# Performance work log

Hardware: AMD Instinct MI355X
Metric: run time of the kernel (lower is better)

## Reference

```python
import jax, jax.numpy as jnp
import numpy as np

B, S, HID = 4, 1024, 4096
H, HKV, D = 32, 8, 128
R = 16
THETA = 10000.0
LORA_SCALE = 1.0


def setup_inputs() -> dict:
    key = jax.random.key(0)
    ks = jax.random.split(key, 13)
    w = 0.02  # init scale for stability
    return {
        "hidden_states": jax.random.normal(ks[0], (B, S, HID), jnp.float32),
        "Wq": jax.random.normal(ks[1], (H * D, HID), jnp.float32) * w,
        "Wk": jax.random.normal(ks[2], (HKV * D, HID), jnp.float32) * w,
        "Wv": jax.random.normal(ks[3], (HKV * D, HID), jnp.float32) * w,
        "Wo": jax.random.normal(ks[4], (HID, H * D), jnp.float32) * w,
        "Aq": jax.random.normal(ks[5], (B, R, HID), jnp.float32) * w,
        "Bq": jax.random.normal(ks[6], (B, H * D, R), jnp.float32) * w,
        "Ak": jax.random.normal(ks[7], (B, R, HID), jnp.float32) * w,
        "Bk": jax.random.normal(ks[8], (B, HKV * D, R), jnp.float32) * w,
        "Av": jax.random.normal(ks[9], (B, R, HID), jnp.float32) * w,
        "Bv": jax.random.normal(ks[10], (B, HKV * D, R), jnp.float32) * w,
        "Ao": jax.random.normal(ks[11], (B, R, H * D), jnp.float32) * w,
        "Bo": jax.random.normal(ks[12], (B, HID, R), jnp.float32) * w,
    }


def _lora(x, A, Bm):
    # per-request (batched) LoRA: x:[B,S,in], A:[B,r,in], Bm:[B,out,r]
    t = jnp.einsum("bsi,bri->bsr", x, A)
    return jnp.einsum("bsr,bor->bso", t, Bm) * LORA_SCALE


def _rope_tables(seq_len, head_dim, theta):
    inv_freq = 1.0 / (theta ** (jnp.arange(0, head_dim, 2, dtype=jnp.float32) / head_dim))
    ang = jnp.arange(seq_len, dtype=jnp.float32)[:, None] * inv_freq[None, :]  # [S, D/2]
    return jnp.cos(ang), jnp.sin(ang)


def _apply_rope(x, cos, sin):
    # x: [B,S,h,D]; cos/sin: [S,D/2]
    x1, x2 = jnp.split(x, 2, axis=-1)
    c = cos[None, :, None, :]
    s = sin[None, :, None, :]
    return jnp.concatenate([x1 * c - x2 * s, x2 * c + x1 * s], axis=-1)


def reference(hidden_states, Wq, Wk, Wv, Wo, Aq, Bq, Ak, Bk, Av, Bv, Ao, Bo):
    x = hidden_states
    # base projections + batched LoRA deltas (apply_lora_weight_kvq)
    q = x @ Wq.T + _lora(x, Aq, Bq)                 # [B,S,H*D]
    k = x @ Wk.T + _lora(x, Ak, Bk)                 # [B,S,HKV*D]
    v = x @ Wv.T + _lora(x, Av, Bv)

    q = q.reshape(B, S, H, D)
    k = k.reshape(B, S, HKV, D)
    v = v.reshape(B, S, HKV, D)

    cos, sin = _rope_tables(S, D, THETA)
    q = _apply_rope(q, cos, sin)
    k = _apply_rope(k, cos, sin)

    # GQA: repeat kv heads to match q heads
    rep = H // HKV
    k = jnp.repeat(k, rep, axis=2)                  # [B,S,H,D]
    v = jnp.repeat(v, rep, axis=2)

    scores = jnp.einsum("bqhd,bkhd->bhqk", q, k) / jnp.sqrt(jnp.float32(D))
    causal = jnp.tril(jnp.ones((S, S), dtype=bool))
    scores = jnp.where(causal[None, None], scores, jnp.finfo(scores.dtype).min)
    probs = jax.nn.softmax(scores, axis=-1)
    attn_raw = jnp.einsum("bhqk,bkhd->bqhd", probs, v).reshape(B, S, H * D)

    # out projection + batched LoRA on attn (apply_lora_weight_attn uses attn_raw)
    out = attn_raw @ Wo.T + _lora(attn_raw, Ao, Bo)  # [B,S,HID]
    return out
```

## Files before the change

kernel.cpp:

```cpp
#include <hip/hip_runtime.h>

typedef unsigned short u16;
typedef __attribute__((ext_vector_type(8))) short short8;
typedef __attribute__((ext_vector_type(4))) float f32x4;

#define BB 4
#define SS 1024
#define HIDN 4096
#define HH 32
#define HKV 8
#define DD 128
#define RR 16
#define MM (BB * SS)
#define NQKV 6144

__device__ __forceinline__ u16 f2bf(float f) {
    unsigned u = __builtin_bit_cast(unsigned, f);
    unsigned r = u + 0x7FFFu + ((u >> 16) & 1u);
    return (u16)(r >> 16);
}
__device__ __forceinline__ float bf2f(u16 u) {
    unsigned v = ((unsigned)u) << 16;
    return __builtin_bit_cast(float, v);
}
__device__ __forceinline__ void glds16(const u16* g, u16* l) {
    __builtin_amdgcn_global_load_lds((const __attribute__((address_space(1))) unsigned int*)g,
                                     (__attribute__((address_space(3))) unsigned int*)l, 16, 0, 0);
}

__global__ void zero_kernel(float* __restrict__ p, int n) {
    int i = blockIdx.x * blockDim.x + threadIdx.x;
    if (i < n) p[i] = 0.f;
}

__global__ void cast_kernel(const float* __restrict__ src, u16* __restrict__ dst, int n4) {
    int i = blockIdx.x * blockDim.x + threadIdx.x;
    int stride = gridDim.x * blockDim.x;
    for (; i < n4; i += stride) {
        float4 v = reinterpret_cast<const float4*>(src)[i];
        ushort4 o;
        o.x = f2bf(v.x); o.y = f2bf(v.y); o.z = f2bf(v.z); o.w = f2bf(v.w);
        reinterpret_cast<ushort4*>(dst)[i] = o;
    }
}

__global__ void cast_lora_a(const float* __restrict__ src, u16* __restrict__ dst,
                            int perB4, int dstStrideU16, int n4) {
    int i = blockIdx.x * blockDim.x + threadIdx.x;
    int stride = gridDim.x * blockDim.x;
    for (; i < n4; i += stride) {
        int b = i / perB4;
        int w4 = i - b * perB4;
        float4 v = reinterpret_cast<const float4*>(src)[i];
        ushort4 o;
        o.x = f2bf(v.x); o.y = f2bf(v.y); o.z = f2bf(v.z); o.w = f2bf(v.w);
        reinterpret_cast<ushort4*>(dst + (size_t)b * dstStrideU16)[w4] = o;
    }
}

template <int NT>
__global__ __launch_bounds__(256) void lora_mfma(
        const u16* __restrict__ Xb, const u16* __restrict__ Ab, float* __restrict__ T) {
    const int N = NT * 16;
    __shared__ __attribute__((aligned(16))) u16 Xls[128 * 32];
    __shared__ __attribute__((aligned(16))) u16 Als[NT * 16 * 32];
    int tid = threadIdx.x;
    int wave = tid >> 6, lane = tid & 63;
    int quad = lane >> 4, l15 = lane & 15;
    int m0 = blockIdx.y * 128;
    int b = m0 >> 10;
    int k0base = blockIdx.x * (HIDN / 4);
    const u16* Abb = Ab + (size_t)b * N * HIDN;
    f32x4 acc[2][NT] = {};
    int r0 = tid >> 2;
    int c0 = (tid & 3) * 8;
    for (int k0 = k0base; k0 < k0base + HIDN / 4; k0 += 32) {
        *(uint4*)&Xls[r0 * 32 + c0]        = *(const uint4*)&Xb[(size_t)(m0 + r0) * HIDN + k0 + c0];
        *(uint4*)&Xls[(r0 + 64) * 32 + c0] = *(const uint4*)&Xb[(size_t)(m0 + r0 + 64) * HIDN + k0 + c0];
        if (tid < NT * 16 * 4)
            *(uint4*)&Als[r0 * 32 + c0] = *(const uint4*)&Abb[(size_t)r0 * HIDN + k0 + c0];
        __syncthreads();
        short8 xf[2], af[NT];
#pragma unroll
        for (int mi = 0; mi < 2; mi++)
            xf[mi] = *(const short8*)&Xls[(wave * 32 + mi * 16 + l15) * 32 + quad * 8];
#pragma unroll
        for (int nt = 0; nt < NT; nt++)
            af[nt] = *(const short8*)&Als[(nt * 16 + l15) * 32 + quad * 8];
#pragma unroll
        for (int mi = 0; mi < 2; mi++)
#pragma unroll
            for (int nt = 0; nt < NT; nt++)
                acc[mi][nt] = __builtin_amdgcn_mfma_f32_16x16x32_bf16(xf[mi], af[nt], acc[mi][nt], 0, 0, 0);
        __syncthreads();
    }
#pragma unroll
    for (int mi = 0; mi < 2; mi++)
#pragma unroll
        for (int nt = 0; nt < NT; nt++)
#pragma unroll
            for (int r = 0; r < 4; r++) {
                int row = m0 + wave * 32 + mi * 16 + quad * 4 + r;
                atomicAdd(&T[(size_t)row * N + nt * 16 + l15], acc[mi][nt][r]);
            }
}

__global__ __launch_bounds__(256) void gemm_fused(
        const u16* __restrict__ Xb, const u16* __restrict__ Wb,
        const float* __restrict__ T, int tstride,
        const float* __restrict__ Bl0, const float* __restrict__ Bl1, const float* __restrict__ Bl2,
        int ns0, int ns1, int ns2, int secb0, int secb1,
        void* __restrict__ outp, int Nout, int out_f32) {
    const int K = HIDN;
    __shared__ __attribute__((aligned(16))) u16 Als[128 * 32];
    __shared__ __attribute__((aligned(16))) u16 Bls[128 * 32];
    int tid = threadIdx.x;
    int wave = tid >> 6, lane = tid & 63;
    int quad = lane >> 4, l15 = lane & 15;
    int wm = wave >> 1, wn = wave & 1;
    int m0 = blockIdx.y * 128, n0 = blockIdx.x * 128;
    int b = m0 >> 10;

    int sec = (n0 >= secb0) + (n0 >= secb1);
    const float* Blp = (sec == 0) ? Bl0 : ((sec == 1) ? Bl1 : Bl2);
    int nsec = (sec == 0) ? ns0 : ((sec == 1) ? ns1 : ns2);
    int colbase = (sec == 0) ? 0 : ((sec == 1) ? secb0 : secb1);
    int toff = sec * 16;
    const float* BlB = Blp + (size_t)b * nsec * RR;

    f32x4 acc[4][4] = {};
    int arow = wave * 32 + (lane >> 2);
    int achunk = ((lane & 3) ^ ((lane >> 3) & 3)) * 8;
    const u16* gA0 = &Xb[(size_t)(m0 + arow) * K + achunk];
    const u16* gA1 = gA0 + (size_t)16 * K;
    const u16* gB0 = &Wb[(size_t)(n0 + arow) * K + achunk];
    const u16* gB1 = gB0 + (size_t)16 * K;
    u16* lA0 = &Als[wave * 32 * 32];
    u16* lA1 = &Als[(wave * 32 + 16) * 32];
    u16* lB0 = &Bls[wave * 32 * 32];
    u16* lB1 = &Bls[(wave * 32 + 16) * 32];
    int sel = ((l15 >> 1) & 3);

    auto compute = [&]() {
        short8 af[4], bfr[4];
#pragma unroll
        for (int mi = 0; mi < 4; mi++)
            af[mi] = *(const short8*)&Als[(wm * 64 + mi * 16 + l15) * 32 + ((quad ^ sel) * 8)];
#pragma unroll
        for (int ni = 0; ni < 4; ni++)
            bfr[ni] = *(const short8*)&Bls[(wn * 64 + ni * 16 + l15) * 32 + ((quad ^ sel) * 8)];
#pragma unroll
        for (int mi = 0; mi < 4; mi++)
#pragma unroll
            for (int ni = 0; ni < 4; ni++)
                acc[mi][ni] = __builtin_amdgcn_mfma_f32_16x16x32_bf16(af[mi], bfr[ni], acc[mi][ni], 0, 0, 0);
    };

    for (int k0 = 0; k0 < K; k0 += 32) {
        glds16(gA0 + k0, lA0);
        glds16(gA1 + k0, lA1);
        glds16(gB0 + k0, lB0);
        glds16(gB1 + k0, lB1);
        __syncthreads();
        compute();
        __syncthreads();
    }

    {
        int r = tid >> 1;
        int s = (r >> 1) & 3;
        short8 z = {0, 0, 0, 0, 0, 0, 0, 0};
        if ((tid & 1) == 0) {
            const float* Tr = &T[(size_t)(m0 + r) * tstride + toff];
            short8 c0v, c1v;
#pragma unroll
            for (int e = 0; e < 4; e++) {
                c0v[e]     = (short)f2bf(Tr[e]);
                c0v[e + 4] = (short)f2bf(Tr[4 + e]);
                c1v[e]     = (short)f2bf(Tr[8 + e]);
                c1v[e + 4] = (short)f2bf(Tr[12 + e]);
            }
            *(short8*)&Als[r * 32 + (0 ^ s) * 8] = c0v;
            *(short8*)&Als[r * 32 + (1 ^ s) * 8] = c1v;
            *(short8*)&Als[r * 32 + (2 ^ s) * 8] = z;
            *(short8*)&Als[r * 32 + (3 ^ s) * 8] = z;
        } else {
            const float* Br = &BlB[(size_t)(n0 - colbase + r) * RR];
            short8 c0v, c1v;
#pragma unroll
            for (int e = 0; e < 4; e++) {
                c0v[e]     = (short)f2bf(Br[e]);
                c0v[e + 4] = (short)f2bf(Br[4 + e]);
                c1v[e]     = (short)f2bf(Br[8 + e]);
                c1v[e + 4] = (short)f2bf(Br[12 + e]);
            }
            *(short8*)&Bls[r * 32 + (0 ^ s) * 8] = c0v;
            *(short8*)&Bls[r * 32 + (1 ^ s) * 8] = c1v;
            *(short8*)&Bls[r * 32 + (2 ^ s) * 8] = z;
            *(short8*)&Bls[r * 32 + (3 ^ s) * 8] = z;
        }
    }
    __syncthreads();
    compute();

#pragma unroll
    for (int mi = 0; mi < 4; mi++) {
#pragma unroll
        for (int r = 0; r < 4; r++) {
            int row = m0 + wm * 64 + mi * 16 + quad * 4 + r;
#pragma unroll
            for (int ni = 0; ni < 4; ni++) {
                int col = n0 + wn * 64 + ni * 16 + l15;
                float v = acc[mi][ni][r];
                if (out_f32) ((float*)outp)[(size_t)row * Nout + col] = v;
                else         ((u16*)outp)[(size_t)row * Nout + col]  = f2bf(v);
            }
        }
    }
}

__global__ void rope_kernel(u16* __restrict__ x, int lognh, int rowstride, int total) {
    int idx = blockIdx.x * 256 + threadIdx.x;
    if (idx >= total) return;
    int d = idx & 63;
    int t = idx >> 6;
    int h = t & ((1 << lognh) - 1);
    int row = t >> lognh;
    int pos = row & (SS - 1);
    size_t base = (size_t)row * rowstride + h * DD;
    float inv = __expf(-(float)d * (9.210340371976184f / 64.0f));
    float ang = (float)pos * inv;
    float c = cosf(ang), s = sinf(ang);
    float x1 = bf2f(x[base + d]);
    float x2 = bf2f(x[base + 64 + d]);
    x[base + d]      = f2bf(x1 * c - x2 * s);
    x[base + 64 + d] = f2bf(x2 * c + x1 * s);
}

#define KLD 136
#define VTLD 72
#define PLD 72
__global__ __launch_bounds__(256) void flash_kernel(
        const u16* __restrict__ Q, const u16* __restrict__ Kx, const u16* __restrict__ V,
        u16* __restrict__ Oa, int qs, int kvs) {
    __shared__ __attribute__((aligned(16))) u16 Kls[64 * KLD];
    __shared__ __attribute__((aligned(16))) u16 Vt[128 * VTLD];
    __shared__ __attribute__((aligned(16))) u16 Pls[4 * 32 * PLD];
    int tid = threadIdx.x;
    int wave = tid >> 6, lane = tid & 63;
    int quad = lane >> 4, l15 = lane & 15;
    int blk = blockIdx.x;
    int qt = 7 - (blk >> 7);
    int h  = blk & 31;
    int b  = (blk >> 5) & 3;
    int hkv = h >> 2;
    int q0 = qt * 128;
    const float scale = 0.08838834764831845f;

    short8 qf[2][4];
#pragma unroll
    for (int mi = 0; mi < 2; mi++) {
        int qrow = q0 + (wave + 4 * mi) * 16 + l15;
        const u16* qp = Q + (size_t)(b * SS + qrow) * qs + h * DD;
#pragma unroll
        for (int kt = 0; kt < 4; kt++) qf[mi][kt] = *(const short8*)&qp[kt * 32 + quad * 8];
    }

    f32x4 oacc[2][8] = {};
    float mrow[2][4], lrow[2][4];
#pragma unroll
    for (int mi = 0; mi < 2; mi++)
#pragma unroll
        for (int r = 0; r < 4; r++) { mrow[mi][r] = -3.0e38f; lrow[mi][r] = 0.f; }

    int krow = tid >> 2;
    int kc   = (tid & 3) * 32;
    int vp   = tid >> 3;
    int vc   = (tid & 7) * 16;

    int nkb = (q0 >> 6) + 2;
    for (int ib = 0; ib < nkb; ib++) {
        int kb = ib * 64;
        const u16* kg = Kx + (size_t)(b * SS + kb + krow) * kvs + hkv * DD + kc;
#pragma unroll
        for (int j = 0; j < 4; j++)
            *(uint4*)&Kls[krow * KLD + kc + j * 8] = *(const uint4*)&kg[j * 8];
        const u16* vg0 = V + (size_t)(b * SS + kb + 2 * vp) * kvs + hkv * DD + vc;
        const u16* vg1 = vg0 + kvs;
#pragma unroll
        for (int j = 0; j < 2; j++) {
            uint4 a4 = *(const uint4*)&vg0[j * 8];
            uint4 b4 = *(const uint4*)&vg1[j * 8];
            const u16* ap = (const u16*)&a4;
            const u16* bp = (const u16*)&b4;
#pragma unroll
            for (int e = 0; e < 8; e++) {
                unsigned pk = (unsigned)ap[e] | ((unsigned)bp[e] << 16);
                *(unsigned*)&Vt[(size_t)(vc + j * 8 + e) * VTLD + 2 * vp] = pk;
            }
        }
        __syncthreads();

        f32x4 sa[2][4] = {};
#pragma unroll
        for (int nt = 0; nt < 4; nt++) {
            short8 kf[4];
#pragma unroll
            for (int kt = 0; kt < 4; kt++)
                kf[kt] = *(const short8*)&Kls[(nt * 16 + l15) * KLD + kt * 32 + quad * 8];
#pragma unroll
            for (int mi = 0; mi < 2; mi++)
#pragma unroll
                for (int kt = 0; kt < 4; kt++)
                    sa[mi][nt] = __builtin_amdgcn_mfma_f32_16x16x32_bf16(qf[mi][kt], kf[kt], sa[mi][nt], 0, 0, 0);
        }

#pragma unroll
        for (int mi = 0; mi < 2; mi++) {
#pragma unroll
            for (int r = 0; r < 4; r++) {
                int qpos = q0 + (wave + 4 * mi) * 16 + quad * 4 + r;
                float s[4];
#pragma unroll
                for (int nt = 0; nt < 4; nt++) {
                    float v = sa[mi][nt][r] * scale;
                    int kpos = kb + nt * 16 + l15;
                    s[nt] = (kpos > qpos) ? -3.0e38f : v;
                }
                float mx = fmaxf(fmaxf(s[0], s[1]), fmaxf(s[2], s[3]));
#pragma unroll
                for (int off = 1; off < 16; off <<= 1) mx = fmaxf(mx, __shfl_xor(mx, off, 64));
                float mnew = fmaxf(mrow[mi][r], mx);
                float alpha = __expf(mrow[mi][r] - mnew);
                mrow[mi][r] = mnew;
                float sum = 0.f;
#pragma unroll
                for (int nt = 0; nt < 4; nt++) {
                    float e = __expf(s[nt] - mnew);
                    sum += e;
                    Pls[wave * (32 * PLD) + (mi * 16 + quad * 4 + r) * PLD + nt * 16 + l15] = f2bf(e);
                }
#pragma unroll
                for (int off = 1; off < 16; off <<= 1) sum += __shfl_xor(sum, off, 64);
                lrow[mi][r] = lrow[mi][r] * alpha + sum;
#pragma unroll
                for (int dt = 0; dt < 8; dt++) oacc[mi][dt][r] *= alpha;
            }
        }
        __syncthreads();

#pragma unroll
        for (int kt = 0; kt < 2; kt++) {
            short8 pf[2];
#pragma unroll
            for (int mi = 0; mi < 2; mi++)
                pf[mi] = *(const short8*)&Pls[wave * (32 * PLD) + (mi * 16 + l15) * PLD + kt * 32 + quad * 8];
#pragma unroll
            for (int dt = 0; dt < 8; dt++) {
                short8 vf = *(const short8*)&Vt[(size_t)(dt * 16 + l15) * VTLD + kt * 32 + quad * 8];
#pragma unroll
                for (int mi = 0; mi < 2; mi++)
                    oacc[mi][dt] = __builtin_amdgcn_mfma_f32_16x16x32_bf16(pf[mi], vf, oacc[mi][dt], 0, 0, 0);
            }
        }
        __syncthreads();
    }

#pragma unroll
    for (int mi = 0; mi < 2; mi++)
#pragma unroll
        for (int r = 0; r < 4; r++) {
            float inv = 1.0f / lrow[mi][r];
            int orow = q0 + (wave + 4 * mi) * 16 + quad * 4 + r;
            u16* op = Oa + ((size_t)(b * SS + orow) * HH + h) * DD;
#pragma unroll
            for (int dt = 0; dt < 8; dt++)
                op[dt * 16 + l15] = f2bf(oacc[mi][dt][r] * inv);
        }
}

extern "C" void kernel_launch(void* const* d_in, const int* in_sizes, int n_in,
                              void* d_out, int out_size, void* d_ws, size_t ws_size,
                              hipStream_t stream) {
    const float* X  = (const float*)d_in[0];
    const float* Wq = (const float*)d_in[1];
    const float* Wk = (const float*)d_in[2];
    const float* Wv = (const float*)d_in[3];
    const float* Wo = (const float*)d_in[4];
    const float* Aq = (const float*)d_in[5];
    const float* Bq = (const float*)d_in[6];
    const float* Ak = (const float*)d_in[7];
    const float* Bk = (const float*)d_in[8];
    const float* Av = (const float*)d_in[9];
    const float* Bv = (const float*)d_in[10];
    const float* Ao = (const float*)d_in[11];
    const float* Bo = (const float*)d_in[12];

    char* w = (char*)d_ws;
    auto take = [&](size_t bytes) {
        char* p = w;
        w += (bytes + 255) & ~(size_t)255;
        return p;
    };
    u16*   Xb  = (u16*)  take((size_t)MM * HIDN * 2);
    u16*   Wqb = (u16*)  take((size_t)HIDN * HIDN * 2);
    u16*   Wkb = (u16*)  take((size_t)1024 * HIDN * 2);
    u16*   Wvb = (u16*)  take((size_t)1024 * HIDN * 2);
    u16*   Wob = (u16*)  take((size_t)HIDN * HIDN * 2);
    float* Tcat= (float*)take((size_t)MM * 48 * 4);
    float* To  = (float*)take((size_t)MM * 16 * 4);
    u16*   Acat= (u16*)  take((size_t)BB * 48 * HIDN * 2);
    u16*   Aob = (u16*)  take((size_t)BB * 16 * HIDN * 2);
    u16*   qkv = (u16*)  take((size_t)MM * NQKV * 2);
    u16*   attn = Xb;

    (void)Wkb; (void)Wvb;

    zero_kernel<<<(MM * 64 + 255) / 256, 256, 0, stream>>>(Tcat, MM * 64);

    cast_kernel<<<2048, 256, 0, stream>>>(X,  Xb,  MM * HIDN / 4);
    cast_kernel<<<2048, 256, 0, stream>>>(Wq, Wqb, HIDN * HIDN / 4);
    cast_kernel<<<1024, 256, 0, stream>>>(Wk, Wkb, 1024 * HIDN / 4);
    cast_kernel<<<1024, 256, 0, stream>>>(Wv, Wvb, 1024 * HIDN / 4);
    cast_kernel<<<2048, 256, 0, stream>>>(Wo, Wob, HIDN * HIDN / 4);
    {
        const int perB4 = 16 * HIDN / 4;
        const int n4 = BB * perB4;
        cast_lora_a<<<256, 256, 0, stream>>>(Aq, Acat,             perB4, 48 * HIDN, n4);
        cast_lora_a<<<256, 256, 0, stream>>>(Ak, Acat + 16 * HIDN, perB4, 48 * HIDN, n4);
        cast_lora_a<<<256, 256, 0, stream>>>(Av, Acat + 32 * HIDN, perB4, 48 * HIDN, n4);
        cast_kernel<<<256, 256, 0, stream>>>(Ao, Aob, BB * 16 * HIDN / 4);
    }

    lora_mfma<3><<<dim3(4, 32), 256, 0, stream>>>(Xb, Acat, Tcat);

    gemm_fused<<<dim3(48, 32), 256, 0, stream>>>(
        Xb, Wqb, Tcat, 48, Bq, Bk, Bv, HIDN, 1024, 1024, 4096, 5120,
        (void*)qkv, NQKV, 0);

    rope_kernel<<<(BB * SS * HH * 64 + 255) / 256, 256, 0, stream>>>(qkv,        5, NQKV, BB * SS * HH * 64);
    rope_kernel<<<(BB * SS * HKV * 64 + 255) / 256, 256, 0, stream>>>(qkv + 4096, 3, NQKV, BB * SS * HKV * 64);

    flash_kernel<<<BB * HH * (SS / 128), 256, 0, stream>>>(qkv, qkv + 4096, qkv + 5120, attn, NQKV, NQKV);

    lora_mfma<1><<<dim3(4, 32), 256, 0, stream>>>(attn, Aob, To);

    gemm_fused<<<dim3(32, 32), 256, 0, stream>>>(
        attn, Wob, To, 16, Bo, Bo, Bo, HIDN, HIDN, HIDN, 1 << 30, 1 << 30,
        (void*)d_out, HIDN, 1);
}
```

Measured before the change: 898.3 us.

## Replace 128x128 GEMM with double-buffered 256x256 ping-pong pipelined GEMM

Swaps the projection GEMM for a 512-thread kernel with 256x256 tiles, K-step 64, and double-buffered LDS. Global-to-LDS loads for later K tiles are interleaved across eight phases and gated by vmcnt waits and raw s_barrier. MFMA bursts run at raised wave priority. The goal is to hide memory latency and raise data reuse per tile, at the cost of more LDS and registers and fewer blocks (384 and 256) on the GPU.

```diff
diff --git a/kernel.cpp b/kernel.cpp
--- a/kernel.cpp
+++ b/kernel.cpp
@@ -27,6 +27,9 @@
     __builtin_amdgcn_global_load_lds((const __attribute__((address_space(1))) unsigned int*)g,
                                      (__attribute__((address_space(3))) unsigned int*)l, 16, 0, 0);
 }
+
+#define BAR()    asm volatile("s_barrier" ::: "memory")
+#define VMCNT6() asm volatile("s_waitcnt vmcnt(6)" ::: "memory")
 
 __global__ void zero_kernel(float* __restrict__ p, int n) {
     int i = blockIdx.x * blockDim.x + threadIdx.x;
@@ -105,20 +108,51 @@
             }
 }
 
-__global__ __launch_bounds__(256) void gemm_fused(
+#define GPH(DB, MB, NB, LOADA, LOADB, STG, ENDW) do {                                   \
+    if (LOADA) {                                                                        \
+        _Pragma("unroll") for (int q_ = 0; q_ < 4; q_++) {                              \
+            int row_ = wm * 128 + ((MB) + q_) * 16 + l15; int sw_ = row_ & 7;           \
+            _Pragma("unroll") for (int kk_ = 0; kk_ < 2; kk_++)                         \
+                afr[q_][kk_] = *(const short8*)&As[DB][row_][((kk_ * 4 + quad) ^ sw_) * 8]; \
+        }                                                                               \
+    }                                                                                   \
+    if (LOADB) {                                                                        \
+        _Pragma("unroll") for (int j_ = 0; j_ < 2; j_++) {                              \
+            int row_ = wn * 64 + ((NB) + j_) * 16 + l15; int sw_ = row_ & 7;            \
+            _Pragma("unroll") for (int kk_ = 0; kk_ < 2; kk_++)                         \
+                bfr[(NB) + j_][kk_] = *(const short8*)&Bs[DB][row_][((kk_ * 4 + quad) ^ sw_) * 8]; \
+        }                                                                               \
+    }                                                                                   \
+    STG;                                                                                \
+    BAR();                                                                              \
+    asm volatile("s_waitcnt lgkmcnt(0)" ::: "memory");                                  \
+    __builtin_amdgcn_sched_barrier(0);                                                  \
+    __builtin_amdgcn_s_setprio(1);                                                      \
+    _Pragma("unroll") for (int kk_ = 0; kk_ < 2; kk_++)                                 \
+    _Pragma("unroll") for (int q_ = 0; q_ < 4; q_++)                                    \
+    _Pragma("unroll") for (int j_ = 0; j_ < 2; j_++)                                    \
+        acc[(MB) + q_][(NB) + j_] = __builtin_amdgcn_mfma_f32_16x16x32_bf16(            \
+            afr[q_][kk_], bfr[(NB) + j_][kk_], acc[(MB) + q_][(NB) + j_], 0, 0, 0);     \
+    __builtin_amdgcn_s_setprio(0);                                                      \
+    ENDW;                                                                               \
+    BAR();                                                                              \
+} while (0)
+
+__global__ __launch_bounds__(512, 2) void gemm256(
         const u16* __restrict__ Xb, const u16* __restrict__ Wb,
         const float* __restrict__ T, int tstride,
         const float* __restrict__ Bl0, const float* __restrict__ Bl1, const float* __restrict__ Bl2,
         int ns0, int ns1, int ns2, int secb0, int secb1,
         void* __restrict__ outp, int Nout, int out_f32) {
     const int K = HIDN;
-    __shared__ __attribute__((aligned(16))) u16 Als[128 * 32];
-    __shared__ __attribute__((aligned(16))) u16 Bls[128 * 32];
+    const int NKT = K / 64;
+    __shared__ __attribute__((aligned(16))) u16 As[2][256][64];
+    __shared__ __attribute__((aligned(16))) u16 Bs[2][256][64];
     int tid = threadIdx.x;
     int wave = tid >> 6, lane = tid & 63;
     int quad = lane >> 4, l15 = lane & 15;
-    int wm = wave >> 1, wn = wave & 1;
-    int m0 = blockIdx.y * 128, n0 = blockIdx.x * 128;
+    int wm = wave >> 2, wn = wave & 3;
+    int m0 = blockIdx.y * 256, n0 = blockIdx.x * 256;
     int b = m0 >> 10;
 
     int sec = (n0 >= secb0) + (n0 >= secb1);
@@ -128,92 +162,109 @@
     int toff = sec * 16;
     const float* BlB = Blp + (size_t)b * nsec * RR;
 
-    f32x4 acc[4][4] = {};
-    int arow = wave * 32 + (lane >> 2);
-    int achunk = ((lane & 3) ^ ((lane >> 3) & 3)) * 8;
-    const u16* gA0 = &Xb[(size_t)(m0 + arow) * K + achunk];
-    const u16* gA1 = gA0 + (size_t)16 * K;
-    const u16* gB0 = &Wb[(size_t)(n0 + arow) * K + achunk];
-    const u16* gB1 = gB0 + (size_t)16 * K;
-    u16* lA0 = &Als[wave * 32 * 32];
-    u16* lA1 = &Als[(wave * 32 + 16) * 32];
-    u16* lB0 = &Bls[wave * 32 * 32];
-    u16* lB1 = &Bls[(wave * 32 + 16) * 32];
-    int sel = ((l15 >> 1) & 3);
-
-    auto compute = [&]() {
-        short8 af[4], bfr[4];
-#pragma unroll
-        for (int mi = 0; mi < 4; mi++)
-            af[mi] = *(const short8*)&Als[(wm * 64 + mi * 16 + l15) * 32 + ((quad ^ sel) * 8)];
-#pragma unroll
-        for (int ni = 0; ni < 4; ni++)
-            bfr[ni] = *(const short8*)&Bls[(wn * 64 + ni * 16 + l15) * 32 + ((quad ^ sel) * 8)];
-#pragma unroll
-        for (int mi = 0; mi < 4; mi++)
+    int rlo = lane >> 3;
+    int cch = lane & 7;
+    unsigned offA[4]; int lA[4];
+#pragma unroll
+    for (int q = 0; q < 4; q++) {
+        int rb = ((wave & 4) << 5) + q * 32 + (wave & 3) * 8;
+        int r = rb + rlo;
+        int g = cch ^ (r & 7);
+        offA[q] = (unsigned)((m0 + r) * K + g * 8);
+        lA[q] = rb;
+    }
+    unsigned offB[2][2]; int lB[2][2];
+#pragma unroll
+    for (int h = 0; h < 2; h++)
+#pragma unroll
+        for (int j = 0; j < 2; j++) {
+            int u = wave * 2 + j;
+            int rb = (u >> 2) * 64 + (u & 3) * 8 + h * 32;
+            int r = rb + rlo;
+            int g = cch ^ (r & 7);
+            offB[h][j] = (unsigned)((n0 + r) * K + g * 8);
+            lB[h][j] = rb;
+        }
+
+    auto stA = [&](int db, int q, int kofs) { glds16(Xb + offA[q] + kofs, &As[db][lA[q]][0]); };
+    auto stB = [&](int db, int h, int j, int kofs) { glds16(Wb + offB[h][j] + kofs, &Bs[db][lB[h][j]][0]); };
+
+    f32x4 acc[8][4] = {};
+    short8 afr[4][2];
+    short8 bfr[4][2];
+
+    stA(0, 0, 0); stA(0, 1, 0); stB(0, 0, 0, 0); stB(0, 0, 1, 0);
+    stA(0, 2, 0); stA(0, 3, 0); stB(0, 1, 0, 0); stB(0, 1, 1, 0);
+    stA(1, 0, 64); stA(1, 1, 64); stB(1, 0, 0, 64); stB(1, 0, 1, 64);
+    stA(1, 2, 64); stA(1, 3, 64);
+    VMCNT6();
+    BAR();
+
+    for (int it = 0; it < NKT / 2; ++it) {
+        int t2 = 2 * it + 2, t3 = 2 * it + 3;
+        int k1 = (2 * it + 1) * 64;
+        int k2 = (t2 < NKT ? t2 : NKT - 1) * 64;
+        int k3 = (t3 < NKT ? t3 : NKT - 1) * 64;
+
+        GPH(0, 0, 0, 1, 1, { stB(1, 1, 0, k1); stB(1, 1, 1, k1); }, );
+        GPH(0, 0, 2, 0, 1, { stA(0, 0, k2); stA(0, 1, k2); }, );
+        GPH(0, 4, 0, 1, 0, { stB(0, 0, 0, k2); stB(0, 0, 1, k2); }, );
+        GPH(0, 4, 2, 0, 0, { stA(0, 2, k2); stA(0, 3, k2); }, VMCNT6());
+        GPH(1, 0, 0, 1, 1, { stB(0, 1, 0, k2); stB(0, 1, 1, k2); }, );
+        GPH(1, 0, 2, 0, 1, { stA(1, 0, k3); stA(1, 1, k3); }, );
+        GPH(1, 4, 0, 1, 0, { stB(1, 0, 0, k3); stB(1, 0, 1, k3); }, );
+        GPH(1, 4, 2, 0, 0, { stA(1, 2, k3); stA(1, 3, k3); }, VMCNT6());
+    }
+
+    __syncthreads();
+    {
+        int r = tid & 255;
+        int sw = r & 7;
+        short8 z = {0, 0, 0, 0, 0, 0, 0, 0};
+        u16* dst; const float* srcp;
+        if (tid < 256) { dst = &As[0][r][0]; srcp = T + (size_t)(m0 + r) * tstride + toff; }
+        else           { dst = &Bs[0][r][0]; srcp = BlB + (size_t)(n0 - colbase + r) * RR; }
+        short8 c0v, c1v;
+#pragma unroll
+        for (int e = 0; e < 8; e++) { c0v[e] = (short)f2bf(srcp[e]); c1v[e] = (short)f2bf(srcp[8 + e]); }
+        *(short8*)&dst[(0 ^ sw) * 8] = c0v;
+        *(short8*)&dst[(1 ^ sw) * 8] = c1v;
+#pragma unroll
+        for (int g = 2; g < 8; g++) *(short8*)&dst[(g ^ sw) * 8] = z;
+    }
+    __syncthreads();
+    {
+        short8 bt[4];
+#pragma unroll
+        for (int ni = 0; ni < 4; ni++) {
+            int row = wn * 64 + ni * 16 + l15; int sw = row & 7;
+            bt[ni] = *(const short8*)&Bs[0][row][(quad ^ sw) * 8];
+        }
+#pragma unroll
+        for (int mi = 0; mi < 8; mi++) {
+            int row = wm * 128 + mi * 16 + l15; int sw = row & 7;
+            short8 at = *(const short8*)&As[0][row][(quad ^ sw) * 8];
 #pragma unroll
             for (int ni = 0; ni < 4; ni++)
-                acc[mi][ni] = __builtin_amdgcn_mfma_f32_16x16x32_bf16(af[mi], bfr[ni], acc[mi][ni], 0, 0, 0);
-    };
-
-    for (int k0 = 0; k0 < K; k0 += 32) {
-        glds16(gA0 + k0, lA0);
-        glds16(gA1 + k0, lA1);
-        glds16(gB0 + k0, lB0);
-        glds16(gB1 + k0, lB1);
-        __syncthreads();
-        compute();
-        __syncthreads();
-    }
-
-    {
-        int r = tid >> 1;
-        int s = (r >> 1) & 3;
-        short8 z = {0, 0, 0, 0, 0, 0, 0, 0};
-        if ((tid & 1) == 0) {
-            const float* Tr = &T[(size_t)(m0 + r) * tstride + toff];
-            short8 c0v, c1v;
-#pragma unroll
-            for (int e = 0; e < 4; e++) {
-                c0v[e]     = (short)f2bf(Tr[e]);
-                c0v[e + 4] = (short)f2bf(Tr[4 + e]);
-                c1v[e]     = (short)f2bf(Tr[8 + e]);
-                c1v[e + 4] = (short)f2bf(Tr[12 + e]);
-            }
-            *(short8*)&Als[r * 32 + (0 ^ s) * 8] = c0v;
-            *(short8*)&Als[r * 32 + (1 ^ s) * 8] = c1v;
-            *(short8*)&Als[r * 32 + (2 ^ s) * 8] = z;
-            *(short8*)&Als[r * 32 + (3 ^ s) * 8] = z;
-        } else {
-            const float* Br = &BlB[(size_t)(n0 - colbase + r) * RR];
-            short8 c0v, c1v;
-#pragma unroll
-            for (int e = 0; e < 4; e++) {
-                c0v[e]     = (short)f2bf(Br[e]);
-                c0v[e + 4] = (short)f2bf(Br[4 + e]);
-                c1v[e]     = (short)f2bf(Br[8 + e]);
-                c1v[e + 4] = (short)f2bf(Br[12 + e]);
-            }
-            *(short8*)&Bls[r * 32 + (0 ^ s) * 8] = c0v;
-            *(short8*)&Bls[r * 32 + (1 ^ s) * 8] = c1v;
-            *(short8*)&Bls[r * 32 + (2 ^ s) * 8] = z;
-            *(short8*)&Bls[r * 32 + (3 ^ s) * 8] = z;
-        }
-    }
-    __syncthreads();
-    compute();
-
-#pragma unroll
-    for (int mi = 0; mi < 4; mi++) {
+                acc[mi][ni] = __builtin_amdgcn_mfma_f32_16x16x32_bf16(at, bt[ni], acc[mi][ni], 0, 0, 0);
+        }
+    }
+
+#pragma unroll
+    for (int mi = 0; mi < 8; mi++) {
 #pragma unroll
         for (int r = 0; r < 4; r++) {
-            int row = m0 + wm * 64 + mi * 16 + quad * 4 + r;
-#pragma unroll
-            for (int ni = 0; ni < 4; ni++) {
-                int col = n0 + wn * 64 + ni * 16 + l15;
-                float v = acc[mi][ni][r];
-                if (out_f32) ((float*)outp)[(size_t)row * Nout + col] = v;
-                else         ((u16*)outp)[(size_t)row * Nout + col]  = f2bf(v);
+            int row = m0 + wm * 128 + mi * 16 + quad * 4 + r;
+            if (out_f32) {
+                float* op = (float*)outp;
+#pragma unroll
+                for (int ni = 0; ni < 4; ni++)
+                    op[(size_t)row * Nout + n0 + wn * 64 + ni * 16 + l15] = acc[mi][ni][r];
+            } else {
+                u16* op = (u16*)outp;
+#pragma unroll
+                for (int ni = 0; ni < 4; ni++)
+                    op[(size_t)row * Nout + n0 + wn * 64 + ni * 16 + l15] = f2bf(acc[mi][ni][r]);
             }
         }
     }
@@ -434,7 +485,7 @@
 
     lora_mfma<3><<<dim3(4, 32), 256, 0, stream>>>(Xb, Acat, Tcat);
 
-    gemm_fused<<<dim3(48, 32), 256, 0, stream>>>(
+    gemm256<<<dim3(24, 16), 512, 0, stream>>>(
         Xb, Wqb, Tcat, 48, Bq, Bk, Bv, HIDN, 1024, 1024, 4096, 5120,
         (void*)qkv, NQKV, 0);
 
@@ -445,7 +496,7 @@
 
     lora_mfma<1><<<dim3(4, 32), 256, 0, stream>>>(attn, Aob, To);
 
-    gemm_fused<<<dim3(32, 32), 256, 0, stream>>>(
+    gemm256<<<dim3(16, 16), 512, 0, stream>>>(
         attn, Wob, To, 16, Bo, Bo, Bo, HIDN, HIDN, HIDN, 1 << 30, 1 << 30,
         (void*)d_out, HIDN, 1);
 }
```

Measured after the change: 910.2 us. Within noise of the previous version (+1.3%).

## Triple-buffer GEMM LDS tiles with async prefetch and manual waitcnt barriers

Applied to the files above, without the earlier changes.

Replaces the single-buffered load/sync/compute loop in the fused projection GEMM with a three-stage LDS ring buffer. Global-to-LDS loads are issued two stages ahead, and completion is tracked with explicit vmcnt waits and raw s_barrier. Fragments are read into registers before the barrier so the buffer can be refilled while the MFMAs run, and setprio raises priority around the MFMA block. This hides global load latency that was previously fully exposed. The cost is triple the LDS footprint, which may reduce occupancy, plus reliance on hand-written waitcnt counts being correct.

```diff
diff --git a/kernel.cpp b/kernel.cpp
--- a/kernel.cpp
+++ b/kernel.cpp
@@ -27,6 +27,11 @@
     __builtin_amdgcn_global_load_lds((const __attribute__((address_space(1))) unsigned int*)g,
                                      (__attribute__((address_space(3))) unsigned int*)l, 16, 0, 0);
 }
+
+#define BAR()    asm volatile("s_barrier" ::: "memory")
+#define VMCNT8() asm volatile("s_waitcnt vmcnt(8)" ::: "memory")
+#define VMCNT4() asm volatile("s_waitcnt vmcnt(4)" ::: "memory")
+#define VMCNT0() asm volatile("s_waitcnt vmcnt(0)" ::: "memory")
 
 __global__ void zero_kernel(float* __restrict__ p, int n) {
     int i = blockIdx.x * blockDim.x + threadIdx.x;
@@ -105,6 +110,30 @@
             }
 }
 
+#define GITER(BUF, KSTAGE, DOSTAGE, WAIT) do {                                           \
+    short8 af_[4], bf_[4];                                                               \
+    _Pragma("unroll") for (int mi_ = 0; mi_ < 4; mi_++)                                  \
+        af_[mi_] = *(const short8*)&Als[BUF][(wm * 64 + mi_ * 16 + l15) * 32 + ((quad ^ sel) * 8)]; \
+    _Pragma("unroll") for (int ni_ = 0; ni_ < 4; ni_++)                                  \
+        bf_[ni_] = *(const short8*)&Bls[BUF][(wn * 64 + ni_ * 16 + l15) * 32 + ((quad ^ sel) * 8)]; \
+    asm volatile("s_waitcnt lgkmcnt(0)" ::: "memory");                                   \
+    __builtin_amdgcn_sched_barrier(0);                                                   \
+    BAR();                                                                               \
+    if (DOSTAGE) {                                                                       \
+        glds16(gA0 + (KSTAGE), &Als[BUF][wave * 32 * 32]);                               \
+        glds16(gA1 + (KSTAGE), &Als[BUF][(wave * 32 + 16) * 32]);                        \
+        glds16(gB0 + (KSTAGE), &Bls[BUF][wave * 32 * 32]);                               \
+        glds16(gB1 + (KSTAGE), &Bls[BUF][(wave * 32 + 16) * 32]);                        \
+    }                                                                                    \
+    __builtin_amdgcn_s_setprio(1);                                                       \
+    _Pragma("unroll") for (int mi_ = 0; mi_ < 4; mi_++)                                  \
+    _Pragma("unroll") for (int ni_ = 0; ni_ < 4; ni_++)                                  \
+        acc[mi_][ni_] = __builtin_amdgcn_mfma_f32_16x16x32_bf16(af_[mi_], bf_[ni_], acc[mi_][ni_], 0, 0, 0); \
+    __builtin_amdgcn_s_setprio(0);                                                       \
+    WAIT;                                                                                \
+    BAR();                                                                               \
+} while (0)
+
 __global__ __launch_bounds__(256) void gemm_fused(
         const u16* __restrict__ Xb, const u16* __restrict__ Wb,
         const float* __restrict__ T, int tstride,
@@ -112,8 +141,8 @@
         int ns0, int ns1, int ns2, int secb0, int secb1,
         void* __restrict__ outp, int Nout, int out_f32) {
     const int K = HIDN;
-    __shared__ __attribute__((aligned(16))) u16 Als[128 * 32];
-    __shared__ __attribute__((aligned(16))) u16 Bls[128 * 32];
+    __shared__ __attribute__((aligned(16))) u16 Als[3][128 * 32];
+    __shared__ __attribute__((aligned(16))) u16 Bls[3][128 * 32];
     int tid = threadIdx.x;
     int wave = tid >> 6, lane = tid & 63;
     int quad = lane >> 4, l15 = lane & 15;
@@ -135,37 +164,30 @@
     const u16* gA1 = gA0 + (size_t)16 * K;
     const u16* gB0 = &Wb[(size_t)(n0 + arow) * K + achunk];
     const u16* gB1 = gB0 + (size_t)16 * K;
-    u16* lA0 = &Als[wave * 32 * 32];
-    u16* lA1 = &Als[(wave * 32 + 16) * 32];
-    u16* lB0 = &Bls[wave * 32 * 32];
-    u16* lB1 = &Bls[(wave * 32 + 16) * 32];
     int sel = ((l15 >> 1) & 3);
 
-    auto compute = [&]() {
-        short8 af[4], bfr[4];
-#pragma unroll
-        for (int mi = 0; mi < 4; mi++)
-            af[mi] = *(const short8*)&Als[(wm * 64 + mi * 16 + l15) * 32 + ((quad ^ sel) * 8)];
-#pragma unroll
-        for (int ni = 0; ni < 4; ni++)
-            bfr[ni] = *(const short8*)&Bls[(wn * 64 + ni * 16 + l15) * 32 + ((quad ^ sel) * 8)];
-#pragma unroll
-        for (int mi = 0; mi < 4; mi++)
-#pragma unroll
-            for (int ni = 0; ni < 4; ni++)
-                acc[mi][ni] = __builtin_amdgcn_mfma_f32_16x16x32_bf16(af[mi], bfr[ni], acc[mi][ni], 0, 0, 0);
-    };
-
-    for (int k0 = 0; k0 < K; k0 += 32) {
-        glds16(gA0 + k0, lA0);
-        glds16(gA1 + k0, lA1);
-        glds16(gB0 + k0, lB0);
-        glds16(gB1 + k0, lB1);
-        __syncthreads();
-        compute();
-        __syncthreads();
-    }
-
+#pragma unroll
+    for (int p = 0; p < 3; p++) {
+        glds16(gA0 + p * 32, &Als[p][wave * 32 * 32]);
+        glds16(gA1 + p * 32, &Als[p][(wave * 32 + 16) * 32]);
+        glds16(gB0 + p * 32, &Bls[p][wave * 32 * 32]);
+        glds16(gB1 + p * 32, &Bls[p][(wave * 32 + 16) * 32]);
+    }
+    VMCNT8();
+    BAR();
+
+    int buf = 0;
+    int kst = 96;
+    for (int t = 0; t < 125; ++t) {
+        GITER(buf, kst, 1, VMCNT8());
+        buf = (buf == 2) ? 0 : buf + 1;
+        kst += 32;
+    }
+    GITER(buf, 0, 0, VMCNT4());  buf = (buf == 2) ? 0 : buf + 1;
+    GITER(buf, 0, 0, VMCNT0());  buf = (buf == 2) ? 0 : buf + 1;
+    GITER(buf, 0, 0, );
+
+    __syncthreads();
     {
         int r = tid >> 1;
         int s = (r >> 1) & 3;
@@ -180,10 +202,10 @@
                 c1v[e]     = (short)f2bf(Tr[8 + e]);
                 c1v[e + 4] = (short)f2bf(Tr[12 + e]);
             }
-            *(short8*)&Als[r * 32 + (0 ^ s) * 8] = c0v;
-            *(short8*)&Als[r * 32 + (1 ^ s) * 8] = c1v;
-            *(short8*)&Als[r * 32 + (2 ^ s) * 8] = z;
-            *(short8*)&Als[r * 32 + (3 ^ s) * 8] = z;
+            *(short8*)&Als[0][r * 32 + (0 ^ s) * 8] = c0v;
+            *(short8*)&Als[0][r * 32 + (1 ^ s) * 8] = c1v;
+            *(short8*)&Als[0][r * 32 + (2 ^ s) * 8] = z;
+            *(short8*)&Als[0][r * 32 + (3 ^ s) * 8] = z;
         } else {
             const float* Br = &BlB[(size_t)(n0 - colbase + r) * RR];
             short8 c0v, c1v;
@@ -194,14 +216,27 @@
                 c1v[e]     = (short)f2bf(Br[8 + e]);
                 c1v[e + 4] = (short)f2bf(Br[12 + e]);
             }
-            *(short8*)&Bls[r * 32 + (0 ^ s) * 8] = c0v;
-            *(short8*)&Bls[r * 32 + (1 ^ s) * 8] = c1v;
-            *(short8*)&Bls[r * 32 + (2 ^ s) * 8] = z;
-            *(short8*)&Bls[r * 32 + (3 ^ s) * 8] = z;
+            *(short8*)&Bls[0][r * 32 + (0 ^ s) * 8] = c0v;
+            *(short8*)&Bls[0][r * 32 + (1 ^ s) * 8] = c1v;
+            *(short8*)&Bls[0][r * 32 + (2 ^ s) * 8] = z;
+            *(short8*)&Bls[0][r * 32 + (3 ^ s) * 8] = z;
         }
     }
     __syncthreads();
-    compute();
+    {
+        short8 af[4], bfr[4];
+#pragma unroll
+        for (int mi = 0; mi < 4; mi++)
+            af[mi] = *(const short8*)&Als[0][(wm * 64 + mi * 16 + l15) * 32 + ((quad ^ sel) * 8)];
+#pragma unroll
+        for (int ni = 0; ni < 4; ni++)
+            bfr[ni] = *(const short8*)&Bls[0][(wn * 64 + ni * 16 + l15) * 32 + ((quad ^ sel) * 8)];
+#pragma unroll
+        for (int mi = 0; mi < 4; mi++)
+#pragma unroll
+            for (int ni = 0; ni < 4; ni++)
+                acc[mi][ni] = __builtin_amdgcn_mfma_f32_16x16x32_bf16(af[mi], bfr[ni], acc[mi][ni], 0, 0, 0);
+    }
 
 #pragma unroll
     for (int mi = 0; mi < 4; mi++) {
```

Result: no change. 915.6 us (+1.9%).
